# Optimization experiments

Measured on AMD Instinct MI355X. Metric: run time of the kernel, lower is better.

Reference implementation:

```python
import jax, jax.numpy as jnp
import numpy as np

B, L, D = 16, 512, 768   # batch, seq_len, hidden_size
H = 12                   # encoder attention heads (self_attention_scores)
K = 128                  # num_preserved_tokens
U, NH = 256, 4           # router attention num_units / num_heads


def setup_inputs() -> dict:
    key = jax.random.key(0)
    ks = jax.random.split(key, 8)
    hidden_states = jax.random.normal(ks[0], (B, L, D), dtype=jnp.float32)
    u = jax.random.uniform(ks[1], (B, 1, 1, L))
    attention_mask = jnp.where(u < 0.9, 0.0, -10000.0).astype(jnp.float32)
    self_attention_scores = jax.random.normal(ks[2], (B, H, L, L), dtype=jnp.float32)
    Wq = jax.random.normal(ks[3], (U, D), dtype=jnp.float32) * 0.02
    Wk = jax.random.normal(ks[4], (U, D), dtype=jnp.float32) * 0.02
    Wv = jax.random.normal(ks[5], (U, D), dtype=jnp.float32) * 0.02
    Wo = jax.random.normal(ks[6], (D, U), dtype=jnp.float32) * 0.02
    bo = jnp.zeros((D,), dtype=jnp.float32)
    return {"hidden_states": hidden_states, "attention_mask": attention_mask,
            "self_attention_scores": self_attention_scores,
            "Wq": Wq, "Wk": Wk, "Wv": Wv, "Wo": Wo, "bo": bo}


def reference(hidden_states, attention_mask, self_attention_scores, Wq, Wk, Wv, Wo, bo):
    # sentence summary: softmax over additive mask -> weighted token average
    att = jax.nn.softmax(attention_mask, axis=-1)            # [B,1,1,L]
    sentences = jnp.einsum('bql,bld->bqd', att[:, 0], hidden_states)  # [B,1,D]

    key_padding_mask = attention_mask[:, 0, 0, :] < -10.0    # [B,L] True = masked

    # MyMultiHeadAttention(query=sentences, key=value=hidden_states)
    hd = U // NH
    q = jnp.einsum('bqd,ud->bqu', sentences, Wq)             # [B,1,U]
    k = jnp.einsum('bld,ud->blu', hidden_states, Wk)         # [B,L,U]
    v = jnp.einsum('bld,ud->blu', hidden_states, Wv)         # [B,L,U]
    qh = q.reshape(B, 1, NH, hd).transpose(2, 0, 1, 3)       # [h,B,1,hd]
    kh = k.reshape(B, L, NH, hd).transpose(2, 0, 1, 3)       # [h,B,L,hd]
    vh = v.reshape(B, L, NH, hd).transpose(2, 0, 1, 3)       # [h,B,L,hd]
    # NOTE: original scales by key_dim**0.5 = hidden_size**0.5 (not head dim)
    scores = jnp.einsum('hbqd,hbkd->hbqk', qh, kh) / (D ** 0.5)  # [h,B,1,L]
    scores = jnp.where(key_padding_mask[None, :, None, :], -jnp.inf, scores)
    probs = jax.nn.softmax(scores, axis=-1)
    out_h = jnp.einsum('hbqk,hbkd->hbqd', probs, vh)         # [h,B,1,hd]
    out = out_h.transpose(1, 2, 0, 3).reshape(B, 1, U)       # concat heads
    new_token = jnp.einsum('bqu,du->bqd', out, Wo) + bo      # [B,1,D]

    class_token = hidden_states[:, :1, :]                    # [B,1,D]

    # importance: mean over heads, sum over query positions -> [B,L]
    importance = self_attention_scores.mean(axis=1).sum(axis=1)
    top_idx = jax.lax.top_k(importance, K)[1]                # [B,K]
    # boolean-mask gather preserves original token order -> sort indices
    sorted_idx = jnp.sort(top_idx, axis=-1)                  # [B,K]
    preserved_tokens = jnp.take_along_axis(hidden_states, sorted_idx[:, :, None], axis=1)  # [B,K,D]
    preserved_mask = jnp.take_along_axis(attention_mask[:, 0, 0, :], sorted_idx, axis=1)
    preserved_mask = preserved_mask.reshape(B, 1, 1, K)

    zmask = jnp.zeros((B, 1, 1, 1), dtype=attention_mask.dtype)
    final_token = jnp.concatenate([class_token, preserved_tokens, new_token], axis=1)  # [B,K+2,D]
    final_attention_mask = jnp.concatenate([zmask, preserved_mask, zmask], axis=-1)    # [B,1,1,K+2]
    return final_token, final_attention_mask
```

## Files before the change

### kernel.cpp

```cpp
#include <hip/hip_runtime.h>
#include <math.h>

#define B_ 16
#define L_ 512
#define D_ 768
#define H_ 12
#define K_ 128
#define U_ 256
#define NH_ 4
#define HD_ 64
#define OUTROWS_ 130
#define IMP_G_ 96

__device__ __forceinline__ float blk_max768(float v, float* red, int t) {
  __syncthreads();
  #pragma unroll
  for (int o = 32; o > 0; o >>= 1) v = fmaxf(v, __shfl_down(v, o, 64));
  if ((t & 63) == 0) red[t >> 6] = v;
  __syncthreads();
  if (t == 0) {
    float r = red[0];
    #pragma unroll
    for (int w = 1; w < 12; ++w) r = fmaxf(r, red[w]);
    red[0] = r;
  }
  __syncthreads();
  return red[0];
}

__device__ __forceinline__ float blk_sum768(float v, float* red, int t) {
  __syncthreads();
  #pragma unroll
  for (int o = 32; o > 0; o >>= 1) v += __shfl_down(v, o, 64);
  if ((t & 63) == 0) red[t >> 6] = v;
  __syncthreads();
  if (t == 0) {
    float r = 0.f;
    #pragma unroll
    for (int w = 0; w < 12; ++w) r += red[w];
    red[0] = r;
  }
  __syncthreads();
  return red[0];
}

__global__ __launch_bounds__(256) void importance_kernel(
    const float* __restrict__ scores, float* __restrict__ part) {
  const int b = blockIdx.y, chunk = blockIdx.x, t = threadIdx.x;
  const int qcol = t & 127;
  const int rhalf = t >> 7;
  const float4* base = (const float4*)scores +
      ((size_t)(b * (H_ * L_) + chunk * 128 + rhalf)) * 128 + qcol;
  float4 a = make_float4(0.f, 0.f, 0.f, 0.f);
  #pragma unroll 8
  for (int r = 0; r < 64; ++r) {
    float4 v = base[(size_t)r * 256];
    a.x += v.x; a.y += v.y; a.z += v.z; a.w += v.w;
  }
  const float s = 1.0f / 12.0f;
  float4 o = make_float4(a.x * s, a.y * s, a.z * s, a.w * s);
  ((float4*)part)[((size_t)b * IMP_G_ + chunk * 2 + rhalf) * 128 + qcol] = o;
}

__global__ __launch_bounds__(768) void sent_kernel(
    const float* __restrict__ hidden, const float* __restrict__ mask,
    float* __restrict__ sent_part) {
  __shared__ float att[L_];
  __shared__ float red[16];
  const int b = blockIdx.x, chunk = blockIdx.y, t = threadIdx.x;
  float m = (t < L_) ? mask[b * L_ + t] : -INFINITY;
  float mx = blk_max768(m, red, t);
  float e = (t < L_) ? expf(m - mx) : 0.f;
  float se = blk_sum768(e, red, t);
  if (t < L_) att[t] = e / se;
  __syncthreads();
  const int l0 = chunk * 32;
  const float* hp = hidden + ((size_t)b * L_ + l0) * D_ + t;
  float acc = 0.f;
  #pragma unroll 8
  for (int l = 0; l < 32; ++l) acc += att[l0 + l] * hp[(size_t)l * D_];
  sent_part[((size_t)b * 16 + chunk) * D_ + t] = acc;
}

__global__ __launch_bounds__(768) void qproj_topk_kernel(
    const float* __restrict__ sent_part, const float* __restrict__ Wq,
    const float* __restrict__ Wk, float* __restrict__ wqe,
    const float* __restrict__ part, const float* __restrict__ mask,
    const float* __restrict__ hidden, float* __restrict__ out0,
    float* __restrict__ out1) {
  __shared__ float s[D_];
  __shared__ float qvh[HD_];
  __shared__ float v[L_];
  __shared__ int lidx[K_];
  __shared__ int wcnt[12];
  const int t = threadIdx.x;
  const int wave = t >> 6, lane = t & 63;

  if (blockIdx.x < 64) {
    const int b = blockIdx.x >> 2, h = blockIdx.x & 3;
    {
      const float* sp = sent_part + (size_t)b * 16 * D_ + t;
      float a = 0.f;
      #pragma unroll
      for (int c = 0; c < 16; ++c) a += sp[(size_t)c * D_];
      s[t] = a;
    }
    __syncthreads();
    for (int u = wave; u < HD_; u += 12) {
      const float* wr = Wq + (size_t)(h * HD_ + u) * D_;
      float acc = 0.f;
      #pragma unroll
      for (int k = 0; k < 12; ++k) {
        const int d = lane + (k << 6);
        acc += wr[d] * s[d];
      }
      #pragma unroll
      for (int o = 32; o > 0; o >>= 1) acc += __shfl_down(acc, o, 64);
      if (lane == 0) qvh[u] = acc;
    }
    __syncthreads();
    {
      float acc = 0.f;
      const float* wk = Wk + (size_t)(h * HD_) * D_ + t;
      #pragma unroll 4
      for (int j = 0; j < HD_; ++j) acc += qvh[j] * wk[(size_t)j * D_];
      wqe[((size_t)b * NH_ + h) * D_ + t] = acc;
    }
  } else {
    const int b = blockIdx.x - 64;
    if (t < L_) {
      const float* pp = part + (size_t)b * IMP_G_ * L_ + t;
      float sum = 0.f;
      #pragma unroll 8
      for (int g = 0; g < IMP_G_; ++g) sum += pp[(size_t)g * L_];
      v[t] = sum;
    }
    __syncthreads();
    bool sel = false;
    if (t < L_) {
      const float mv = v[t];
      int cnt = 0;
      #pragma unroll 8
      for (int j = 0; j < L_; ++j) {
        float o = v[j];
        cnt += (o > mv) || (o == mv && j < t);
      }
      sel = cnt < K_;
    }
    const unsigned long long ball = __ballot(sel);
    if (lane == 0) wcnt[wave] = __popcll(ball);
    __syncthreads();
    int base = 0;
    for (int w = 0; w < wave; ++w) base += wcnt[w];
    const int pos = base + __popcll(ball & ((1ull << lane) - 1ull));
    if (sel) {
      lidx[pos] = t;
      out1[b * OUTROWS_ + 1 + pos] = mask[b * L_ + t];
    }
    if (t == 0) {
      out1[b * OUTROWS_ + 0] = 0.f;
      out1[b * OUTROWS_ + OUTROWS_ - 1] = 0.f;
    }
    __syncthreads();
    const float4* hb4 = (const float4*)(hidden + (size_t)b * L_ * D_);
    float4* ob4 = (float4*)(out0 + (size_t)b * OUTROWS_ * D_);
    const int NG = (K_ + 1) * 192;
    for (int i = t; i < NG; i += 768) {
      const int r = i / 192;
      const int c = i - r * 192;
      const int src = (r == 0) ? 0 : lidx[r - 1];
      ob4[r * 192 + c] = hb4[src * 192 + c];
    }
  }
}

__global__ __launch_bounds__(256) void score_kernel(
    const float* __restrict__ hidden, const float* __restrict__ mask,
    const float* __restrict__ wqe, float* __restrict__ scores) {
  __shared__ float4 wq4[NH_ * 192];
  const int b = blockIdx.x, chunk = blockIdx.y, t = threadIdx.x;
  {
    const float4* wsrc = (const float4*)(wqe + (size_t)b * NH_ * D_);
    for (int i = t; i < NH_ * 192; i += 256) wq4[i] = wsrc[i];
  }
  __syncthreads();
  const int wave = t >> 6, lane = t & 63;
  const float scale = 0.03608439182435161f;
  #pragma unroll
  for (int r = 0; r < 8; ++r) {
    const int l = chunk * 32 + wave * 8 + r;
    const float4* hr4 = (const float4*)(hidden + ((size_t)b * L_ + l) * D_);
    float s0 = 0.f, s1 = 0.f, s2 = 0.f, s3 = 0.f;
    #pragma unroll
    for (int jj = 0; jj < 3; ++jj) {
      const int c = lane + 64 * jj;
      const float4 hv = hr4[c];
      const float4 w0 = wq4[0 * 192 + c];
      const float4 w1 = wq4[1 * 192 + c];
      const float4 w2 = wq4[2 * 192 + c];
      const float4 w3 = wq4[3 * 192 + c];
      s0 += hv.x * w0.x + hv.y * w0.y + hv.z * w0.z + hv.w * w0.w;
      s1 += hv.x * w1.x + hv.y * w1.y + hv.z * w1.z + hv.w * w1.w;
      s2 += hv.x * w2.x + hv.y * w2.y + hv.z * w2.z + hv.w * w2.w;
      s3 += hv.x * w3.x + hv.y * w3.y + hv.z * w3.z + hv.w * w3.w;
    }
    #pragma unroll
    for (int o = 32; o > 0; o >>= 1) {
      s0 += __shfl_down(s0, o, 64);
      s1 += __shfl_down(s1, o, 64);
      s2 += __shfl_down(s2, o, 64);
      s3 += __shfl_down(s3, o, 64);
    }
    if (lane == 0) {
      const bool kp = mask[b * L_ + l] < -10.f;
      float* sp = scores + (size_t)b * NH_ * L_ + l;
      sp[0 * L_] = kp ? -INFINITY : s0 * scale;
      sp[1 * L_] = kp ? -INFINITY : s1 * scale;
      sp[2 * L_] = kp ? -INFINITY : s2 * scale;
      sp[3 * L_] = kp ? -INFINITY : s3 * scale;
    }
  }
}

__global__ __launch_bounds__(768) void ctx_prob_kernel(
    const float* __restrict__ hidden, const float* __restrict__ scores,
    float* __restrict__ ctx_part) {
  __shared__ float pr[NH_][32];
  __shared__ float red[16];
  const int b = blockIdx.x, chunk = blockIdx.y, t = threadIdx.x;
  const int l0 = chunk * 32;
  #pragma unroll
  for (int h = 0; h < NH_; ++h) {
    const float* sp = scores + ((size_t)b * NH_ + h) * L_;
    float val = (t < L_) ? sp[t] : -INFINITY;
    float mx = blk_max768(val, red, t);
    float e = (t < L_) ? expf(val - mx) : 0.f;
    float se = blk_sum768(e, red, t);
    if (t >= l0 && t < l0 + 32) pr[h][t - l0] = e / se;
  }
  __syncthreads();
  const float* hp = hidden + ((size_t)b * L_ + l0) * D_ + t;
  float c0 = 0.f, c1 = 0.f, c2 = 0.f, c3 = 0.f;
  #pragma unroll 8
  for (int l = 0; l < 32; ++l) {
    float hv = hp[(size_t)l * D_];
    c0 += pr[0][l] * hv;
    c1 += pr[1][l] * hv;
    c2 += pr[2][l] * hv;
    c3 += pr[3][l] * hv;
  }
  float* cb = ctx_part + ((size_t)b * 16 + chunk) * NH_ * D_ + t;
  cb[0 * D_] = c0;
  cb[1 * D_] = c1;
  cb[2 * D_] = c2;
  cb[3 * D_] = c3;
}

__global__ __launch_bounds__(768) void outv_kernel(
    const float* __restrict__ ctx_part, const float* __restrict__ Wv,
    float* __restrict__ outv) {
  __shared__ float ch[D_];
  const int b = blockIdx.x, h = blockIdx.y, t = threadIdx.x;
  const int wave = t >> 6, lane = t & 63;
  {
    float a = 0.f;
    #pragma unroll
    for (int c = 0; c < 16; ++c)
      a += ctx_part[(((size_t)b * 16 + c) * NH_ + h) * D_ + t];
    ch[t] = a;
  }
  __syncthreads();
  for (int u = wave; u < HD_; u += 12) {
    const float* wr = Wv + (size_t)(h * HD_ + u) * D_;
    float acc = 0.f;
    #pragma unroll
    for (int k = 0; k < 12; ++k) {
      const int d = lane + (k << 6);
      acc += wr[d] * ch[d];
    }
    #pragma unroll
    for (int o = 32; o > 0; o >>= 1) acc += __shfl_down(acc, o, 64);
    if (lane == 0) outv[b * U_ + h * HD_ + u] = acc;
  }
}

__global__ __launch_bounds__(192) void newtoken_kernel(
    const float* __restrict__ outv, const float* __restrict__ Wo,
    const float* __restrict__ bo, float* __restrict__ out0) {
  __shared__ float4 ov4[64];
  const int b = blockIdx.x, q = blockIdx.y, t = threadIdx.x;
  const int wave = t >> 6, lane = t & 63;
  if (t < 64) ov4[t] = ((const float4*)(outv + b * U_))[t];
  __syncthreads();
  const int dbase = q * 192 + wave * 64;
  const float4 o = ov4[lane];
  for (int i = 0; i < 64; ++i) {
    const int d = dbase + i;
    const float4 w = ((const float4*)(Wo + (size_t)d * U_))[lane];
    float acc = w.x * o.x + w.y * o.y + w.z * o.z + w.w * o.w;
    #pragma unroll
    for (int off = 32; off > 0; off >>= 1) acc += __shfl_down(acc, off, 64);
    if (lane == 0)
      out0[((size_t)b * OUTROWS_ + (OUTROWS_ - 1)) * D_ + d] = bo[d] + acc;
  }
}

extern "C" void kernel_launch(void* const* d_in, const int* in_sizes, int n_in,
                              void* d_out, int out_size, void* d_ws, size_t ws_size,
                              hipStream_t stream) {
  const float* hidden = (const float*)d_in[0];
  const float* mask   = (const float*)d_in[1];
  const float* sas    = (const float*)d_in[2];
  const float* Wq     = (const float*)d_in[3];
  const float* Wk     = (const float*)d_in[4];
  const float* Wv     = (const float*)d_in[5];
  const float* Wo     = (const float*)d_in[6];
  const float* bo     = (const float*)d_in[7];

  float* out0 = (float*)d_out;
  float* out1 = out0 + (size_t)B_ * OUTROWS_ * D_;

  float* part      = (float*)d_ws;
  float* sent_part = part + (size_t)B_ * IMP_G_ * L_;
  float* ctx_part  = sent_part + (size_t)B_ * 16 * D_;
  float* wqe       = ctx_part + (size_t)B_ * 16 * NH_ * D_;
  float* scores    = wqe + (size_t)B_ * NH_ * D_;
  float* outv      = scores + (size_t)B_ * NH_ * L_;

  importance_kernel<<<dim3(48, B_), 256, 0, stream>>>(sas, part);
  sent_kernel<<<dim3(B_, 16), 768, 0, stream>>>(hidden, mask, sent_part);
  qproj_topk_kernel<<<80, 768, 0, stream>>>(sent_part, Wq, Wk, wqe,
                                            part, mask, hidden, out0, out1);
  score_kernel<<<dim3(B_, 16), 256, 0, stream>>>(hidden, mask, wqe, scores);
  ctx_prob_kernel<<<dim3(B_, 16), 768, 0, stream>>>(hidden, scores, ctx_part);
  outv_kernel<<<dim3(B_, NH_), 768, 0, stream>>>(ctx_part, Wv, outv);
  newtoken_kernel<<<dim3(B_, 4), 192, 0, stream>>>(outv, Wo, bo, out0);
}
```

Before: 400.2 us.

## Merge importance and sentence kernels; compute softmax stats in score kernel

Folds the importance reduction and the sentence-summary kernel into a single launch with branch-by-block-index, and recasts the sentence part to 256 threads. The score kernel now emits per-chunk online-softmax max/sum statistics, so the context kernel combines 16 partials instead of running four full-block max/sum reductions over all 512 scores per block. This removes a launch and redundant reductions in exchange for a slightly more complex stats combine and an extra small workspace buffer.

```diff
diff --git a/kernel.cpp b/kernel.cpp
--- a/kernel.cpp
+++ b/kernel.cpp
@@ -12,74 +12,78 @@
 #define OUTROWS_ 130
 #define IMP_G_ 96
 
-__device__ __forceinline__ float blk_max768(float v, float* red, int t) {
+__device__ __forceinline__ float blk_max256(float v, float* red, int t) {
   __syncthreads();
   #pragma unroll
   for (int o = 32; o > 0; o >>= 1) v = fmaxf(v, __shfl_down(v, o, 64));
   if ((t & 63) == 0) red[t >> 6] = v;
   __syncthreads();
   if (t == 0) {
-    float r = red[0];
-    #pragma unroll
-    for (int w = 1; w < 12; ++w) r = fmaxf(r, red[w]);
+    float r = fmaxf(fmaxf(red[0], red[1]), fmaxf(red[2], red[3]));
     red[0] = r;
   }
   __syncthreads();
   return red[0];
 }
 
-__device__ __forceinline__ float blk_sum768(float v, float* red, int t) {
+__device__ __forceinline__ float blk_sum256(float v, float* red, int t) {
   __syncthreads();
   #pragma unroll
   for (int o = 32; o > 0; o >>= 1) v += __shfl_down(v, o, 64);
   if ((t & 63) == 0) red[t >> 6] = v;
   __syncthreads();
-  if (t == 0) {
-    float r = 0.f;
-    #pragma unroll
-    for (int w = 0; w < 12; ++w) r += red[w];
-    red[0] = r;
-  }
+  if (t == 0) red[0] = red[0] + red[1] + red[2] + red[3];
   __syncthreads();
   return red[0];
 }
 
-__global__ __launch_bounds__(256) void importance_kernel(
-    const float* __restrict__ scores, float* __restrict__ part) {
-  const int b = blockIdx.y, chunk = blockIdx.x, t = threadIdx.x;
-  const int qcol = t & 127;
-  const int rhalf = t >> 7;
-  const float4* base = (const float4*)scores +
-      ((size_t)(b * (H_ * L_) + chunk * 128 + rhalf)) * 128 + qcol;
-  float4 a = make_float4(0.f, 0.f, 0.f, 0.f);
-  #pragma unroll 8
-  for (int r = 0; r < 64; ++r) {
-    float4 v = base[(size_t)r * 256];
-    a.x += v.x; a.y += v.y; a.z += v.z; a.w += v.w;
-  }
-  const float s = 1.0f / 12.0f;
-  float4 o = make_float4(a.x * s, a.y * s, a.z * s, a.w * s);
-  ((float4*)part)[((size_t)b * IMP_G_ + chunk * 2 + rhalf) * 128 + qcol] = o;
-}
-
-__global__ __launch_bounds__(768) void sent_kernel(
-    const float* __restrict__ hidden, const float* __restrict__ mask,
+__global__ __launch_bounds__(256) void imp_sent_kernel(
+    const float* __restrict__ scores, const float* __restrict__ hidden,
+    const float* __restrict__ mask, float* __restrict__ part,
     float* __restrict__ sent_part) {
-  __shared__ float att[L_];
-  __shared__ float red[16];
-  const int b = blockIdx.x, chunk = blockIdx.y, t = threadIdx.x;
-  float m = (t < L_) ? mask[b * L_ + t] : -INFINITY;
-  float mx = blk_max768(m, red, t);
-  float e = (t < L_) ? expf(m - mx) : 0.f;
-  float se = blk_sum768(e, red, t);
-  if (t < L_) att[t] = e / se;
-  __syncthreads();
-  const int l0 = chunk * 32;
-  const float* hp = hidden + ((size_t)b * L_ + l0) * D_ + t;
-  float acc = 0.f;
-  #pragma unroll 8
-  for (int l = 0; l < 32; ++l) acc += att[l0 + l] * hp[(size_t)l * D_];
-  sent_part[((size_t)b * 16 + chunk) * D_ + t] = acc;
+  const int b = blockIdx.y, t = threadIdx.x;
+  if (blockIdx.x < 48) {
+    const int chunk = blockIdx.x;
+    const int qcol = t & 127;
+    const int rhalf = t >> 7;
+    const float4* base = (const float4*)scores +
+        ((size_t)(b * (H_ * L_) + chunk * 128 + rhalf)) * 128 + qcol;
+    float4 a = make_float4(0.f, 0.f, 0.f, 0.f);
+    #pragma unroll 8
+    for (int r = 0; r < 64; ++r) {
+      float4 v = base[(size_t)r * 256];
+      a.x += v.x; a.y += v.y; a.z += v.z; a.w += v.w;
+    }
+    const float s = 1.0f / 12.0f;
+    float4 o = make_float4(a.x * s, a.y * s, a.z * s, a.w * s);
+    ((float4*)part)[((size_t)b * IMP_G_ + chunk * 2 + rhalf) * 128 + qcol] = o;
+  } else {
+    __shared__ float att[L_];
+    __shared__ float red[4];
+    const int chunk = blockIdx.x - 48;
+    const float m0 = mask[b * L_ + t];
+    const float m1 = mask[b * L_ + 256 + t];
+    float mx = blk_max256(fmaxf(m0, m1), red, t);
+    const float e0 = expf(m0 - mx);
+    const float e1 = expf(m1 - mx);
+    float se = blk_sum256(e0 + e1, red, t);
+    att[t] = e0 / se;
+    att[t + 256] = e1 / se;
+    __syncthreads();
+    const int l0 = chunk * 32;
+    const float* hp = hidden + ((size_t)b * L_ + l0) * D_;
+    float a0 = 0.f, a1 = 0.f, a2 = 0.f;
+    #pragma unroll 8
+    for (int l = 0; l < 32; ++l) {
+      const float av = att[l0 + l];
+      const float* hr = hp + (size_t)l * D_;
+      a0 += av * hr[t];
+      a1 += av * hr[t + 256];
+      a2 += av * hr[t + 512];
+    }
+    float* sp = sent_part + ((size_t)b * 16 + chunk) * D_;
+    sp[t] = a0; sp[t + 256] = a1; sp[t + 512] = a2;
+  }
 }
 
 __global__ __launch_bounds__(768) void qproj_topk_kernel(
@@ -176,8 +180,10 @@
 
 __global__ __launch_bounds__(256) void score_kernel(
     const float* __restrict__ hidden, const float* __restrict__ mask,
-    const float* __restrict__ wqe, float* __restrict__ scores) {
+    const float* __restrict__ wqe, float* __restrict__ scores,
+    float* __restrict__ stats) {
   __shared__ float4 wq4[NH_ * 192];
+  __shared__ float wstat[4][NH_][2];
   const int b = blockIdx.x, chunk = blockIdx.y, t = threadIdx.x;
   {
     const float4* wsrc = (const float4*)(wqe + (size_t)b * NH_ * D_);
@@ -186,6 +192,8 @@
   __syncthreads();
   const int wave = t >> 6, lane = t & 63;
   const float scale = 0.03608439182435161f;
+  float rm0 = -INFINITY, rm1 = -INFINITY, rm2 = -INFINITY, rm3 = -INFINITY;
+  float rs0 = 0.f, rs1 = 0.f, rs2 = 0.f, rs3 = 0.f;
   #pragma unroll
   for (int r = 0; r < 8; ++r) {
     const int l = chunk * 32 + wave * 8 + r;
@@ -213,30 +221,67 @@
     }
     if (lane == 0) {
       const bool kp = mask[b * L_ + l] < -10.f;
+      const float f0 = kp ? -INFINITY : s0 * scale;
+      const float f1 = kp ? -INFINITY : s1 * scale;
+      const float f2 = kp ? -INFINITY : s2 * scale;
+      const float f3 = kp ? -INFINITY : s3 * scale;
       float* sp = scores + (size_t)b * NH_ * L_ + l;
-      sp[0 * L_] = kp ? -INFINITY : s0 * scale;
-      sp[1 * L_] = kp ? -INFINITY : s1 * scale;
-      sp[2 * L_] = kp ? -INFINITY : s2 * scale;
-      sp[3 * L_] = kp ? -INFINITY : s3 * scale;
-    }
-  }
-}
-
-__global__ __launch_bounds__(768) void ctx_prob_kernel(
+      sp[0 * L_] = f0; sp[1 * L_] = f1; sp[2 * L_] = f2; sp[3 * L_] = f3;
+      if (!kp) {
+        float nm;
+        nm = fmaxf(rm0, f0); rs0 = rs0 * expf(rm0 - nm) + expf(f0 - nm); rm0 = nm;
+        nm = fmaxf(rm1, f1); rs1 = rs1 * expf(rm1 - nm) + expf(f1 - nm); rm1 = nm;
+        nm = fmaxf(rm2, f2); rs2 = rs2 * expf(rm2 - nm) + expf(f2 - nm); rm2 = nm;
+        nm = fmaxf(rm3, f3); rs3 = rs3 * expf(rm3 - nm) + expf(f3 - nm); rm3 = nm;
+      }
+    }
+  }
+  if (lane == 0) {
+    wstat[wave][0][0] = rm0; wstat[wave][0][1] = rs0;
+    wstat[wave][1][0] = rm1; wstat[wave][1][1] = rs1;
+    wstat[wave][2][0] = rm2; wstat[wave][2][1] = rs2;
+    wstat[wave][3][0] = rm3; wstat[wave][3][1] = rs3;
+  }
+  __syncthreads();
+  if (t < NH_) {
+    float M = -INFINITY, S = 0.f;
+    #pragma unroll
+    for (int w = 0; w < 4; ++w) M = fmaxf(M, wstat[w][t][0]);
+    if (M > -INFINITY) {
+      #pragma unroll
+      for (int w = 0; w < 4; ++w)
+        S += wstat[w][t][1] * expf(wstat[w][t][0] - M);
+    }
+    float* st = stats + (((size_t)b * NH_ + t) * 16 + chunk) * 2;
+    st[0] = M; st[1] = S;
+  }
+}
+
+__global__ __launch_bounds__(768) void ctx_kernel(
     const float* __restrict__ hidden, const float* __restrict__ scores,
-    float* __restrict__ ctx_part) {
+    const float* __restrict__ stats, float* __restrict__ ctx_part) {
   __shared__ float pr[NH_][32];
-  __shared__ float red[16];
+  __shared__ float MS[NH_][2];
   const int b = blockIdx.x, chunk = blockIdx.y, t = threadIdx.x;
   const int l0 = chunk * 32;
-  #pragma unroll
-  for (int h = 0; h < NH_; ++h) {
-    const float* sp = scores + ((size_t)b * NH_ + h) * L_;
-    float val = (t < L_) ? sp[t] : -INFINITY;
-    float mx = blk_max768(val, red, t);
-    float e = (t < L_) ? expf(val - mx) : 0.f;
-    float se = blk_sum768(e, red, t);
-    if (t >= l0 && t < l0 + 32) pr[h][t - l0] = e / se;
+  if (t < NH_) {
+    const float* st = stats + ((size_t)b * NH_ + t) * 16 * 2;
+    float M = -INFINITY;
+    #pragma unroll
+    for (int c = 0; c < 16; ++c) M = fmaxf(M, st[c * 2]);
+    float S = 0.f;
+    #pragma unroll
+    for (int c = 0; c < 16; ++c) {
+      const float m_c = st[c * 2];
+      if (m_c > -INFINITY) S += st[c * 2 + 1] * expf(m_c - M);
+    }
+    MS[t][0] = M; MS[t][1] = S;
+  }
+  __syncthreads();
+  if (t < NH_ * 32) {
+    const int h = t >> 5, j = t & 31;
+    const float x = scores[((size_t)b * NH_ + h) * L_ + l0 + j];
+    pr[h][j] = expf(x - MS[h][0]) / MS[h][1];
   }
   __syncthreads();
   const float* hp = hidden + ((size_t)b * L_ + l0) * D_ + t;
@@ -325,14 +370,16 @@
   float* ctx_part  = sent_part + (size_t)B_ * 16 * D_;
   float* wqe       = ctx_part + (size_t)B_ * 16 * NH_ * D_;
   float* scores    = wqe + (size_t)B_ * NH_ * D_;
-  float* outv      = scores + (size_t)B_ * NH_ * L_;
-
-  importance_kernel<<<dim3(48, B_), 256, 0, stream>>>(sas, part);
-  sent_kernel<<<dim3(B_, 16), 768, 0, stream>>>(hidden, mask, sent_part);
+  float* stats     = scores + (size_t)B_ * NH_ * L_;
+  float* outv      = stats + (size_t)B_ * NH_ * 16 * 2;
+
+  imp_sent_kernel<<<dim3(64, B_), 256, 0, stream>>>(sas, hidden, mask,
+                                                    part, sent_part);
   qproj_topk_kernel<<<80, 768, 0, stream>>>(sent_part, Wq, Wk, wqe,
                                             part, mask, hidden, out0, out1);
-  score_kernel<<<dim3(B_, 16), 256, 0, stream>>>(hidden, mask, wqe, scores);
-  ctx_prob_kernel<<<dim3(B_, 16), 768, 0, stream>>>(hidden, scores, ctx_part);
+  score_kernel<<<dim3(B_, 16), 256, 0, stream>>>(hidden, mask, wqe,
+                                                 scores, stats);
+  ctx_kernel<<<dim3(B_, 16), 768, 0, stream>>>(hidden, scores, stats, ctx_part);
   outv_kernel<<<dim3(B_, NH_), 768, 0, stream>>>(ctx_part, Wv, outv);
   newtoken_kernel<<<dim3(B_, 4), 192, 0, stream>>>(outv, Wo, bo, out0);
 }
```

Result: no change. 403.5 us (+0.8%).
